# Kernel optimization log

Measured on AMD Instinct MI355X. Metric: run time of the kernel, lower is better.

Reference implementation:

```python
import jax, jax.numpy as jnp
from jax import lax
import numpy as np

B, T, MEL, H, H2, VOCAB, K, L, TXT = 16, 1000, 80, 512, 256, 80, 5, 2, 200


def _lstm_dir(x, Wih, Whh, b):
    # x: [T, B, D]; torch gate order i, f, g, o
    def step(carry, xt):
        h, c = carry
        g = xt @ Wih.T + h @ Whh.T + b
        i, f, gg, o = jnp.split(g, 4, axis=-1)
        c = jax.nn.sigmoid(f) * c + jax.nn.sigmoid(i) * jnp.tanh(gg)
        h = jax.nn.sigmoid(o) * jnp.tanh(c)
        return (h, c), h
    n = x.shape[1]
    h0 = jnp.zeros((n, Whh.shape[-1]), x.dtype)
    _, hs = lax.scan(step, (h0, h0), x)
    return hs


def _bilstm(x, Wih, Whh, b):
    # Wih: [L, 2, 4*H2, D], Whh: [L, 2, 4*H2, H2], b: [L, 2, 4*H2] (b_ih + b_hh folded)
    for l in range(Wih.shape[0]):
        fwd = _lstm_dir(x, Wih[l, 0], Whh[l, 0], b[l, 0])
        bwd = _lstm_dir(x[::-1], Wih[l, 1], Whh[l, 1], b[l, 1])[::-1]
        x = jnp.concatenate([fwd, bwd], axis=-1)
    return x


def _causal_conv(x, w, bias, pad):
    y = lax.conv_general_dilated(x, w, window_strides=(1,), padding=[(pad, 0)],
                                 dimension_numbers=('NCH', 'OIH', 'NCH'))
    return y + bias[None, :, None]


def _bn(x, g, b, m, v):
    # eval-mode BatchNorm1d over channel dim of [B, C, T]
    return (x - m[None, :, None]) * (g / jnp.sqrt(v + 1e-5))[None, :, None] + b[None, :, None]


def _ln(x, g, b):
    mu = jnp.mean(x, -1, keepdims=True)
    var = jnp.var(x, -1, keepdims=True)
    return (x - mu) / jnp.sqrt(var + 1e-5) * g + b


def _forward(mels, c1w, c1b, bn1g, bn1b, bn1m, bn1v, c2w, c2b, bn2g, bn2b, bn2m, bn2v,
             eWih, eWhh, eb, elng, elnb, cWih, cWhh, cb, ctcW, btlW, lng, lnb,
             dWih, dWhh, db, melW, mel_lengths):
    t = mels.shape[2]
    # norm_spec: spec_min=-12, spec_max=0
    x = (mels + 12.0) / 12.0 * 2.0 - 1.0
    # Conv1dPrenet (causal pads, eval-mode BN)
    y = _bn(_causal_conv(x, c1w, c1b, K - 1), bn1g, bn1b, bn1m, bn1v)
    y = _bn(_causal_conv(y, c2w, c2b, K - 1), bn2g, bn2b, bn2m, bn2v)
    xs = jnp.transpose(y, (2, 0, 1))  # [T, B, H]
    # MelEncoder BiLSTM + LayerNorm -> decoder_input [T, B, H]
    h = _ln(_bilstm(xs, eWih, eWhh, eb), elng, elnb)
    # CTCDecoder
    cx = _bilstm(h, cWih, cWhh, cb)                 # raw LSTM output (returned as ctc_hidden)
    logits = jax.nn.relu(cx) @ ctcW.T               # dropout is identity in eval
    mask = (jnp.arange(t)[:, None] < mel_lengths[None, :]).astype(logits.dtype)[:, :, None]
    log_prob = jax.nn.log_softmax(logits, axis=-1) * mask
    # bottleneck: cat(decoder_input, ctc_hidden) -> linear -> LN
    bh = _ln(jnp.concatenate([h, cx], axis=-1) @ btlW.T, lng, lnb)
    # MELDecoder (note: mel_linear applied to raw LSTM output x, matching source)
    mx = _bilstm(bh, dWih, dWhh, db)
    mel = mx @ melW.T
    mel = (mel + 1.0) / 2.0 * 12.0 - 12.0           # denorm_spec
    return mel, log_prob


def setup_inputs() -> dict:
    key = jax.random.key(0)
    ks = list(jax.random.split(key, 24))
    rn = lambda k, shape, s=0.05: jax.random.normal(k, shape, jnp.float32) * s
    G = 4 * H2
    inp = {
        'mels': jax.random.uniform(ks[0], (B, MEL, T), jnp.float32, -12.0, 0.0),
        'c1w': rn(ks[1], (H, MEL, K)), 'c1b': jnp.zeros((H,), jnp.float32),
        'bn1g': jnp.ones((H,), jnp.float32), 'bn1b': jnp.zeros((H,), jnp.float32),
        'bn1m': jnp.zeros((H,), jnp.float32), 'bn1v': jnp.ones((H,), jnp.float32),
        'c2w': rn(ks[2], (H, H, K)), 'c2b': jnp.zeros((H,), jnp.float32),
        'bn2g': jnp.ones((H,), jnp.float32), 'bn2b': jnp.zeros((H,), jnp.float32),
        'bn2m': jnp.zeros((H,), jnp.float32), 'bn2v': jnp.ones((H,), jnp.float32),
        'eWih': rn(ks[3], (L, 2, G, H)), 'eWhh': rn(ks[4], (L, 2, G, H2)), 'eb': rn(ks[5], (L, 2, G)),
        'elng': jnp.ones((H,), jnp.float32), 'elnb': jnp.zeros((H,), jnp.float32),
        'cWih': rn(ks[6], (L, 2, G, H)), 'cWhh': rn(ks[7], (L, 2, G, H2)), 'cb': rn(ks[8], (L, 2, G)),
        'ctcW': rn(ks[9], (VOCAB, H)),
        'btlW': rn(ks[10], (H, 2 * H)),
        'lng': jnp.ones((H,), jnp.float32), 'lnb': jnp.zeros((H,), jnp.float32),
        'dWih': rn(ks[11], (L, 2, G, H)), 'dWhh': rn(ks[12], (L, 2, G, H2)), 'db': rn(ks[13], (L, 2, G)),
        'melW': rn(ks[14], (MEL, H)),
        'mel_lengths': jnp.full((B,), T, jnp.int32),  # full lengths: pack/pad is identity
        'text_inputs': jax.random.randint(ks[15], (B, TXT), 0, VOCAB),
        'text_lengths': jnp.full((B,), TXT, jnp.int32),
    }
    return inp


def reference(mels, c1w, c1b, bn1g, bn1b, bn1m, bn1v, c2w, c2b, bn2g, bn2b, bn2m, bn2v,
              eWih, eWhh, eb, elng, elnb, cWih, cWhh, cb, ctcW, btlW, lng, lnb,
              dWih, dWhh, db, melW, mel_lengths, text_inputs, text_lengths):
    return _forward(mels, c1w, c1b, bn1g, bn1b, bn1m, bn1v, c2w, c2b, bn2g, bn2b, bn2m, bn2v,
                    eWih, eWhh, eb, elng, elnb, cWih, cWhh, cb, ctcW, btlW, lng, lnb,
                    dWih, dWhh, db, melW, mel_lengths)
```

## Files before the change

kernel.cpp:

```cpp
#include <hip/hip_runtime.h>
#include <hip/hip_fp16.h>


typedef unsigned int u32;
typedef _Float16 h2_t __attribute__((ext_vector_type(2)));
typedef _Float16 f16x8 __attribute__((ext_vector_type(8)));
typedef float f32x4 __attribute__((ext_vector_type(4)));
union U32H2 { u32 u; h2_t h; };

#define T_LEN 1000
#define BATCH 16
#define SROWS (T_LEN * BATCH)

__device__ __forceinline__ float dot2f(u32 a, u32 b, float c) {
#if __has_builtin(__builtin_amdgcn_fdot2)
    U32H2 ua; ua.u = a; U32H2 ub; ub.u = b;
    return __builtin_amdgcn_fdot2(ua.h, ub.h, c, false);
#else
    U32H2 ua; ua.u = a; U32H2 ub; ub.u = b;
    return c + (float)ua.h.x * (float)ub.h.x + (float)ua.h.y * (float)ub.h.y;
#endif
}

__device__ __forceinline__ u32 pack2h(float a, float b) {
    h2_t p; p.x = (_Float16)a; p.y = (_Float16)b;
    U32H2 u; u.h = p; return u.u;
}

__device__ __forceinline__ float fsigm(float x) { return 1.0f / (1.0f + __expf(-x)); }
__device__ __forceinline__ float ftanh_(float x) {
    x = fminf(fmaxf(x, -15.0f), 15.0f);
    float e = __expf(-2.0f * x);
    return (1.0f - e) / (1.0f + e);
}

__global__ void transpose_kernel(const float* __restrict__ src, float* __restrict__ dst,
                                 int R, int C) {
    int total = R * C;
    for (int i = blockIdx.x * blockDim.x + threadIdx.x; i < total; i += gridDim.x * blockDim.x) {
        int r = i / C, c = i - r * C;
        dst[(size_t)c * R + r] = src[i];
    }
}

__global__ void prep_whh_kernel(const float* __restrict__ whh, u32* __restrict__ wp, int total) {
    for (int idx = blockIdx.x * blockDim.x + threadIdx.x; idx < total; idx += gridDim.x * blockDim.x) {
        int q = idx & 3;
        int j = (idx >> 2) & 1023;
        int g = (idx >> 12) & 31;
        int d = (idx >> 17) & 1;
        int l = idx >> 18;
        int k = g * 8 + q * 2;
        const float* s = whh + ((size_t)(l * 2 + d) * 1024 + j) * 256 + k;
        wp[idx] = pack2h(s[0], s[1]);
    }
}

__global__ void pack_b_kernel(const float* __restrict__ src, _Float16* __restrict__ dst,
                              int N, int K, int sn, int sk, int off) {
    int total = N * K;
    int kst = K >> 5;
    for (int idx = blockIdx.x * blockDim.x + threadIdx.x; idx < total; idx += gridDim.x * blockDim.x) {
        int i = idx & 7;
        int lane = (idx >> 3) & 63;
        int rest = idx >> 9;
        int ks = rest % kst;
        int nt = rest / kst;
        int n = nt * 16 + (lane & 15);
        int k = ks * 32 + (lane >> 4) * 8 + i;
        dst[idx] = (_Float16)src[(size_t)n * sn + (size_t)k * sk + off];
    }
}

__global__ __launch_bounds__(256) void conv1_kernel(
    const float* __restrict__ mels, const float* __restrict__ w,
    const float* __restrict__ cbias, const float* __restrict__ bg,
    const float* __restrict__ bb, const float* __restrict__ bm,
    const float* __restrict__ bv, float* __restrict__ y1)
{
    __shared__ float xin[80 * 72];
    int t0 = blockIdx.x * 64;
    int b = blockIdx.y;
    int tid = threadIdx.x;
    for (int idx = tid; idx < 80 * 68; idx += 256) {
        int m = idx / 68, i = idx - m * 68;
        int t = t0 - 4 + i;
        float v = 0.0f;
        if (t >= 0 && t < T_LEN) v = mels[(size_t)(b * 80 + m) * T_LEN + t] * (1.0f / 6.0f) + 1.0f;
        xin[m * 72 + i] = v;
    }
    __syncthreads();
    int tg = tid & 15, cl = tid >> 4;
    for (int pass = 0; pass < 32; ++pass) {
        int c = pass * 16 + cl;
        const float* wc = w + (size_t)c * 400;
        float a0 = 0, a1 = 0, a2 = 0, a3 = 0;
        for (int m = 0; m < 80; ++m) {
            float4 xa = *(const float4*)&xin[m * 72 + tg * 4];
            float4 xb = *(const float4*)&xin[m * 72 + tg * 4 + 4];
            float w0 = wc[m * 5 + 0], w1 = wc[m * 5 + 1], w2 = wc[m * 5 + 2];
            float w3 = wc[m * 5 + 3], w4 = wc[m * 5 + 4];
            a0 += w0 * xa.x + w1 * xa.y + w2 * xa.z + w3 * xa.w + w4 * xb.x;
            a1 += w0 * xa.y + w1 * xa.z + w2 * xa.w + w3 * xb.x + w4 * xb.y;
            a2 += w0 * xa.z + w1 * xa.w + w2 * xb.x + w3 * xb.y + w4 * xb.z;
            a3 += w0 * xa.w + w1 * xb.x + w2 * xb.y + w3 * xb.z + w4 * xb.w;
        }
        float scale = bg[c] * rsqrtf(bv[c] + 1e-5f);
        float shift = (cbias[c] - bm[c]) * scale + bb[c];
        int tb = t0 + tg * 4;
        float* yp = y1 + (size_t)(b * 512 + c) * T_LEN + tb;
        if (tb + 0 < T_LEN) yp[0] = a0 * scale + shift;
        if (tb + 1 < T_LEN) yp[1] = a1 * scale + shift;
        if (tb + 2 < T_LEN) yp[2] = a2 * scale + shift;
        if (tb + 3 < T_LEN) yp[3] = a3 * scale + shift;
    }
}

__global__ __launch_bounds__(256) void relayout_kernel(
    const float* __restrict__ y1, _Float16* __restrict__ dst)
{
    __shared__ float tile[64][65];
    int t0 = blockIdx.x * 64;
    int c0 = blockIdx.y * 64;
    int b = blockIdx.z;
    int tid = threadIdx.x;
#pragma unroll
    for (int q = 0; q < 16; ++q) {
        int lin = tid + q * 256;
        int cl = lin >> 6, tl = lin & 63;
        int t = t0 + tl;
        tile[cl][tl] = (t < T_LEN) ? y1[(size_t)(b * 512 + c0 + cl) * T_LEN + t] : 0.0f;
    }
    __syncthreads();
#pragma unroll
    for (int q = 0; q < 16; ++q) {
        int lin = tid + q * 256;
        int rl = lin >> 6, cc = lin & 63;
        int t = t0 + rl;
        if (t < T_LEN)
            dst[(size_t)(t * BATCH + b) * 512 + c0 + cc] = (_Float16)tile[cc][rl];
    }
}

template<int MODE>
__global__ __launch_bounds__(512, 2) void gemm_mfma(
    const _Float16* __restrict__ A, const _Float16* __restrict__ A2, int K1,
    const uint4* __restrict__ Bp, const float* __restrict__ bias,
    float* __restrict__ C32, _Float16* __restrict__ C16,
    const float* __restrict__ cvb, const float* __restrict__ bg,
    const float* __restrict__ bb, const float* __restrict__ bm,
    const float* __restrict__ bv, int N, int K)
{
    __shared__ _Float16 At[128 * 40];
    const int m0 = blockIdx.x * 128, n0 = blockIdx.y * 128;
    const int tid = threadIdx.x, lane = tid & 63, w = tid >> 6;
    const int wm = w >> 2, wn = w & 3;
    const int srow = tid >> 2, sseg = tid & 3;
    const int ksteps = K >> 5;
    f32x4 acc[4][2];
#pragma unroll
    for (int i = 0; i < 4; ++i) { acc[i][0] = (f32x4)0.0f; acc[i][1] = (f32x4)0.0f; }

    for (int ks = 0; ks < ksteps; ++ks) {
        int k0 = ks << 5;
        uint4 av;
        if (MODE == 1) {
            int kph = k0 >> 9, kk = k0 & 511;
            int rsrc = m0 + srow + (kph - 4) * 16;
            if (rsrc >= 0) av = *(const uint4*)(A + (size_t)rsrc * 512 + kk + sseg * 8);
            else { av.x = av.y = av.z = av.w = 0u; }
        } else {
            int col = k0 + sseg * 8;
            const _Float16* src = (col < K1) ? (A + (size_t)(m0 + srow) * K1 + col)
                                             : (A2 + (size_t)(m0 + srow) * (K - K1) + (col - K1));
            av = *(const uint4*)src;
        }
        __syncthreads();
        *(uint4*)&At[srow * 40 + sseg * 8] = av;
        __syncthreads();

        f16x8 bf[2];
#pragma unroll
        for (int ct = 0; ct < 2; ++ct) {
            int nt = (n0 >> 4) + wn * 2 + ct;
            int bblk = (MODE == 1) ? ((ks >> 4) * 512 + nt * 16 + (ks & 15))
                                   : (nt * ksteps + ks);
            uint4 braw = Bp[(size_t)bblk * 64 + lane];
            bf[ct] = *(f16x8*)&braw;
        }
#pragma unroll
        for (int rt = 0; rt < 4; ++rt) {
            f16x8 af = *(f16x8*)&At[(wm * 64 + rt * 16 + (lane & 15)) * 40 + (lane >> 4) * 8];
            acc[rt][0] = __builtin_amdgcn_mfma_f32_16x16x32_f16(af, bf[0], acc[rt][0], 0, 0, 0);
            acc[rt][1] = __builtin_amdgcn_mfma_f32_16x16x32_f16(af, bf[1], acc[rt][1], 0, 0, 0);
        }
    }

    const int r0 = m0 + wm * 64 + (lane >> 4) * 4;
    const int cb0 = n0 + wn * 32 + (lane & 15);
#pragma unroll
    for (int ct = 0; ct < 2; ++ct) {
        int col = cb0 + ct * 16;
        float badd = 0.0f, sc = 0.0f, sh = 0.0f;
        if (MODE == 0) { if (bias) badd = bias[col]; }
        else {
            sc = bg[col] * rsqrtf(bv[col] + 1e-5f);
            sh = (cvb[col] - bm[col]) * sc + bb[col];
        }
#pragma unroll
        for (int rt = 0; rt < 4; ++rt) {
#pragma unroll
            for (int rr = 0; rr < 4; ++rr) {
                int row = r0 + rt * 16 + rr;
                float v = acc[rt][ct][rr];
                if (MODE == 0) C32[(size_t)row * N + col] = v + badd;
                else           C16[(size_t)row * 512 + col] = (_Float16)(v * sc + sh);
            }
        }
    }
}

#define SCAN_LDS (147456 + 4096 + 512)
__global__ __launch_bounds__(512, 2) void lstm_scan(
    const float* __restrict__ pre, const uint4* __restrict__ WPl,
    float* __restrict__ out32, _Float16* __restrict__ out16)
{
    const int b = blockIdx.x >> 1;
    const int dir = blockIdx.x & 1;
    const int tid = threadIdx.x;
    const int j0 = tid, j1 = tid + 512;

    extern __shared__ char smem[];
    uint4* w_lds = (uint4*)smem;
    float* gates = (float*)(smem + 147456);
    u32* h16 = (u32*)(smem + 147456 + 4096);

    const uint4* wp = WPl + (size_t)dir * 32768;

    for (int i = tid; i < 9216; i += 512) w_lds[i] = wp[i];

    uint4 wr0[21], wr1[21];
#pragma unroll
    for (int i = 0; i < 21; ++i) {
        wr0[i] = wp[(9 + i) * 1024 + j0];
        wr1[i] = wp[(9 + i) * 1024 + j1];
    }
    if (tid < 128) h16[tid] = 0u;
    float c = 0.0f;
    __syncthreads();

    for (int step = 0; step < T_LEN; ++step) {
        int tt = dir ? (T_LEN - 1 - step) : step;
        const float* prow = pre + (size_t)(tt * BATCH + b) * 2048 + (dir << 10);
        float acc0 = prow[j0];
        float acc1 = prow[j1];
        uint4 ws0[2], ws1[2];
#pragma unroll
        for (int i = 0; i < 2; ++i) {
            ws0[i] = wp[(30 + i) * 1024 + j0];
            ws1[i] = wp[(30 + i) * 1024 + j1];
        }
#pragma unroll
        for (int g = 0; g < 9; ++g) {
            uint4 hv = *(const uint4*)&h16[g * 4];
            uint4 w0 = w_lds[g * 1024 + j0];
            uint4 w1 = w_lds[g * 1024 + j1];
            acc0 = dot2f(hv.x, w0.x, acc0); acc0 = dot2f(hv.y, w0.y, acc0);
            acc0 = dot2f(hv.z, w0.z, acc0); acc0 = dot2f(hv.w, w0.w, acc0);
            acc1 = dot2f(hv.x, w1.x, acc1); acc1 = dot2f(hv.y, w1.y, acc1);
            acc1 = dot2f(hv.z, w1.z, acc1); acc1 = dot2f(hv.w, w1.w, acc1);
        }
#pragma unroll
        for (int i = 0; i < 21; ++i) {
            uint4 hv = *(const uint4*)&h16[(9 + i) * 4];
            acc0 = dot2f(hv.x, wr0[i].x, acc0); acc0 = dot2f(hv.y, wr0[i].y, acc0);
            acc0 = dot2f(hv.z, wr0[i].z, acc0); acc0 = dot2f(hv.w, wr0[i].w, acc0);
            acc1 = dot2f(hv.x, wr1[i].x, acc1); acc1 = dot2f(hv.y, wr1[i].y, acc1);
            acc1 = dot2f(hv.z, wr1[i].z, acc1); acc1 = dot2f(hv.w, wr1[i].w, acc1);
        }
#pragma unroll
        for (int i = 0; i < 2; ++i) {
            uint4 hv = *(const uint4*)&h16[(30 + i) * 4];
            acc0 = dot2f(hv.x, ws0[i].x, acc0); acc0 = dot2f(hv.y, ws0[i].y, acc0);
            acc0 = dot2f(hv.z, ws0[i].z, acc0); acc0 = dot2f(hv.w, ws0[i].w, acc0);
            acc1 = dot2f(hv.x, ws1[i].x, acc1); acc1 = dot2f(hv.y, ws1[i].y, acc1);
            acc1 = dot2f(hv.z, ws1[i].z, acc1); acc1 = dot2f(hv.w, ws1[i].w, acc1);
        }
        gates[j0] = acc0;
        gates[j1] = acc1;
        __syncthreads();
        if (tid < 256) {
            float gi = gates[tid], gf = gates[tid + 256];
            float gg = gates[tid + 512], go = gates[tid + 768];
            c = fsigm(gf) * c + fsigm(gi) * ftanh_(gg);
            float h = fsigm(go) * ftanh_(c);
            size_t orow = (size_t)(tt * BATCH + b) * 512 + dir * 256 + tid;
            if (out32) out32[orow] = h;
            if (out16) out16[orow] = (_Float16)h;
            float hn = __shfl_xor(h, 1);
            if ((tid & 1) == 0) h16[tid >> 1] = pack2h(h, hn);
        }
        __syncthreads();
    }
}

__global__ __launch_bounds__(256) void ln_kernel(
    const float* __restrict__ in, const float* __restrict__ g,
    const float* __restrict__ b, _Float16* __restrict__ out, int rows)
{
    int row = blockIdx.x * 4 + (threadIdx.x >> 6);
    if (row >= rows) return;
    int lane = threadIdx.x & 63;
    const float4* x = (const float4*)(in + (size_t)row * 512);
    float4 v0 = x[lane * 2], v1 = x[lane * 2 + 1];
    float s = v0.x + v0.y + v0.z + v0.w + v1.x + v1.y + v1.z + v1.w;
    float sq = v0.x * v0.x + v0.y * v0.y + v0.z * v0.z + v0.w * v0.w
             + v1.x * v1.x + v1.y * v1.y + v1.z * v1.z + v1.w * v1.w;
#pragma unroll
    for (int m = 1; m < 64; m <<= 1) {
        s += __shfl_xor(s, m);
        sq += __shfl_xor(sq, m);
    }
    float mu = s * (1.0f / 512.0f);
    float var = sq * (1.0f / 512.0f) - mu * mu;
    float rs = rsqrtf(var + 1e-5f);
    const float4* g4 = (const float4*)g;
    const float4* b4 = (const float4*)b;
    f16x8 r;
    float vv[8] = {v0.x, v0.y, v0.z, v0.w, v1.x, v1.y, v1.z, v1.w};
    float4 gg0 = g4[lane * 2], gg1 = g4[lane * 2 + 1];
    float4 bb0 = b4[lane * 2], bb1 = b4[lane * 2 + 1];
    float gA[8] = {gg0.x, gg0.y, gg0.z, gg0.w, gg1.x, gg1.y, gg1.z, gg1.w};
    float bA[8] = {bb0.x, bb0.y, bb0.z, bb0.w, bb1.x, bb1.y, bb1.z, bb1.w};
#pragma unroll
    for (int q = 0; q < 8; ++q) r[q] = (_Float16)((vv[q] - mu) * rs * gA[q] + bA[q]);
    *(f16x8*)&out[(size_t)row * 512 + lane * 8] = r;
}

__global__ __launch_bounds__(128) void ctc_head_kernel(
    const float* __restrict__ cx, const float* __restrict__ ctcWt,
    const int* __restrict__ lens, float* __restrict__ out)
{
    int r = blockIdx.x;
    int t = r / BATCH, b = r - t * BATCH;
    int tid = threadIdx.x;
    __shared__ float xr[512];
    __shared__ float red[128];
    for (int i = tid; i < 512; i += 128) xr[i] = fmaxf(cx[(size_t)r * 512 + i], 0.0f);
    __syncthreads();
    float logit = 0.0f;
    if (tid < 80) {
#pragma unroll 8
        for (int k = 0; k < 512; ++k) logit += xr[k] * ctcWt[k * 80 + tid];
    }
    red[tid] = (tid < 80) ? logit : -1e30f;
    __syncthreads();
    for (int off = 64; off > 0; off >>= 1) {
        if (tid < off) red[tid] = fmaxf(red[tid], red[tid + off]);
        __syncthreads();
    }
    float m = red[0];
    __syncthreads();
    red[tid] = (tid < 80) ? __expf(logit - m) : 0.0f;
    __syncthreads();
    for (int off = 64; off > 0; off >>= 1) {
        if (tid < off) red[tid] += red[tid + off];
        __syncthreads();
    }
    float lsum = __logf(red[0]);
    if (tid < 80) {
        float lp = logit - m - lsum;
        out[(size_t)r * 80 + tid] = (t < lens[b]) ? lp : 0.0f;
    }
}

__global__ __launch_bounds__(128) void mel_head_kernel(
    const float* __restrict__ mx, const float* __restrict__ melWt,
    float* __restrict__ out)
{
    int r = blockIdx.x;
    int tid = threadIdx.x;
    __shared__ float xr[512];
    for (int i = tid; i < 512; i += 128) xr[i] = mx[(size_t)r * 512 + i];
    __syncthreads();
    if (tid < 80) {
        float acc = 0.0f;
#pragma unroll 8
        for (int k = 0; k < 512; ++k) acc += xr[k] * melWt[k * 80 + tid];
        out[(size_t)r * 80 + tid] = acc * 6.0f - 6.0f;
    }
}

extern "C" void kernel_launch(void* const* d_in, const int* in_sizes, int n_in,
                              void* d_out, int out_size, void* d_ws, size_t ws_size,
                              hipStream_t stream) {
    const float* mels = (const float*)d_in[0];
    const float* c1w = (const float*)d_in[1];
    const float* c1b = (const float*)d_in[2];
    const float* bn1g = (const float*)d_in[3];
    const float* bn1b = (const float*)d_in[4];
    const float* bn1m = (const float*)d_in[5];
    const float* bn1v = (const float*)d_in[6];
    const float* c2w = (const float*)d_in[7];
    const float* c2b = (const float*)d_in[8];
    const float* bn2g = (const float*)d_in[9];
    const float* bn2b = (const float*)d_in[10];
    const float* bn2m = (const float*)d_in[11];
    const float* bn2v = (const float*)d_in[12];
    const float* eWih = (const float*)d_in[13];
    const float* eWhh = (const float*)d_in[14];
    const float* eb   = (const float*)d_in[15];
    const float* elng = (const float*)d_in[16];
    const float* elnb = (const float*)d_in[17];
    const float* cWih = (const float*)d_in[18];
    const float* cWhh = (const float*)d_in[19];
    const float* cb   = (const float*)d_in[20];
    const float* ctcW = (const float*)d_in[21];
    const float* btlW = (const float*)d_in[22];
    const float* lng  = (const float*)d_in[23];
    const float* lnb  = (const float*)d_in[24];
    const float* dWih = (const float*)d_in[25];
    const float* dWhh = (const float*)d_in[26];
    const float* db   = (const float*)d_in[27];
    const float* melW = (const float*)d_in[28];
    const int* mel_lengths = (const int*)d_in[29];

    float* out = (float*)d_out;
    float* ws = (float*)d_ws;

    float* preB = ws;
    float* s32  = ws + 32768000;
    _Float16* f0 = (_Float16*)(ws + 40960000);
    _Float16* f1 = f0 + 8192000;
    _Float16* f2 = f1 + 8192000;
    _Float16* f3 = f2 + 8192000;
    _Float16* BP    = f3 + 8192000;
    _Float16* BPbtl = BP + 6ull * 1048576;
    _Float16* BPcv  = BPbtl + 524288;
    u32* wpAll = (u32*)(BPcv + 5ull * 262144);
    float* ctcT = (float*)(wpAll + 6ull * 262144);
    float* melT = ctcT + 40960;

    (void)hipFuncSetAttribute((const void*)lstm_scan,
                              hipFuncAttributeMaxDynamicSharedMemorySize, SCAN_LDS);

    transpose_kernel<<<160, 256, 0, stream>>>(ctcW, ctcT, 80, 512);
    transpose_kernel<<<160, 256, 0, stream>>>(melW, melT, 80, 512);
    prep_whh_kernel<<<2048, 256, 0, stream>>>(eWhh, wpAll + 0ull * 262144, 2 * 262144);
    prep_whh_kernel<<<2048, 256, 0, stream>>>(cWhh, wpAll + 2ull * 262144, 2 * 262144);
    prep_whh_kernel<<<2048, 256, 0, stream>>>(dWhh, wpAll + 4ull * 262144, 2 * 262144);
    for (int l = 0; l < 2; ++l) {
        pack_b_kernel<<<1024, 256, 0, stream>>>(eWih + (size_t)l * 1048576,
                                                BP + (size_t)(0 + l) * 1048576, 2048, 512, 512, 1, 0);
        pack_b_kernel<<<1024, 256, 0, stream>>>(cWih + (size_t)l * 1048576,
                                                BP + (size_t)(2 + l) * 1048576, 2048, 512, 512, 1, 0);
        pack_b_kernel<<<1024, 256, 0, stream>>>(dWih + (size_t)l * 1048576,
                                                BP + (size_t)(4 + l) * 1048576, 2048, 512, 512, 1, 0);
    }
    pack_b_kernel<<<1024, 256, 0, stream>>>(btlW, BPbtl, 512, 1024, 1024, 1, 0);
    for (int kph = 0; kph < 5; ++kph)
        pack_b_kernel<<<512, 256, 0, stream>>>(c2w, BPcv + (size_t)kph * 262144,
                                               512, 512, 2560, 5, kph);

    conv1_kernel<<<dim3(16, 16), 256, 0, stream>>>(mels, c1w, c1b, bn1g, bn1b, bn1m, bn1v, s32);
    relayout_kernel<<<dim3(16, 8, 16), 256, 0, stream>>>(s32, f0);
    gemm_mfma<1><<<dim3(125, 4), 512, 0, stream>>>(f0, nullptr, 0, (const uint4*)BPcv, nullptr,
                                                   nullptr, f1, c2b, bn2g, bn2b, bn2m, bn2v, 512, 2560);

    dim3 gN2048(125, 16), gN512(125, 4);
    const uint4* BPu = (const uint4*)BP;
    gemm_mfma<0><<<gN2048, 512, 0, stream>>>(f1, nullptr, 512, BPu + 0ull * 131072, eb,
                                             preB, nullptr, nullptr, nullptr, nullptr, nullptr, nullptr, 2048, 512);
    lstm_scan<<<32, 512, SCAN_LDS, stream>>>(preB, (const uint4*)(wpAll + 0ull * 262144), nullptr, f2);
    gemm_mfma<0><<<gN2048, 512, 0, stream>>>(f2, nullptr, 512, BPu + 1ull * 131072, eb + 2048,
                                             preB, nullptr, nullptr, nullptr, nullptr, nullptr, nullptr, 2048, 512);
    lstm_scan<<<32, 512, SCAN_LDS, stream>>>(preB, (const uint4*)(wpAll + 1ull * 262144), s32, nullptr);
    ln_kernel<<<4000, 256, 0, stream>>>(s32, elng, elnb, f2, SROWS);
    gemm_mfma<0><<<gN2048, 512, 0, stream>>>(f2, nullptr, 512, BPu + 2ull * 131072, cb,
                                             preB, nullptr, nullptr, nullptr, nullptr, nullptr, nullptr, 2048, 512);
    lstm_scan<<<32, 512, SCAN_LDS, stream>>>(preB, (const uint4*)(wpAll + 2ull * 262144), nullptr, f3);
    gemm_mfma<0><<<gN2048, 512, 0, stream>>>(f3, nullptr, 512, BPu + 3ull * 131072, cb + 2048,
                                             preB, nullptr, nullptr, nullptr, nullptr, nullptr, nullptr, 2048, 512);
    lstm_scan<<<32, 512, SCAN_LDS, stream>>>(preB, (const uint4*)(wpAll + 3ull * 262144), s32, f1);
    ctc_head_kernel<<<SROWS, 128, 0, stream>>>(s32, ctcT, mel_lengths, out + (size_t)SROWS * 80);
    gemm_mfma<0><<<gN512, 512, 0, stream>>>(f2, f1, 512, (const uint4*)BPbtl, nullptr,
                                            preB, nullptr, nullptr, nullptr, nullptr, nullptr, nullptr, 512, 1024);
    ln_kernel<<<4000, 256, 0, stream>>>(preB, lng, lnb, f3, SROWS);
    gemm_mfma<0><<<gN2048, 512, 0, stream>>>(f3, nullptr, 512, BPu + 4ull * 131072, db,
                                             preB, nullptr, nullptr, nullptr, nullptr, nullptr, nullptr, 2048, 512);
    lstm_scan<<<32, 512, SCAN_LDS, stream>>>(preB, (const uint4*)(wpAll + 4ull * 262144), nullptr, f2);
    gemm_mfma<0><<<gN2048, 512, 0, stream>>>(f2, nullptr, 512, BPu + 5ull * 131072, db + 2048,
                                             preB, nullptr, nullptr, nullptr, nullptr, nullptr, nullptr, 2048, 512);
    lstm_scan<<<32, 512, SCAN_LDS, stream>>>(preB, (const uint4*)(wpAll + 5ull * 262144), s32, nullptr);
    mel_head_kernel<<<SROWS, 128, 0, stream>>>(s32, melT, out);
}
```

Baseline: 12.48 ms.

## Cache LSTM recurrent weights in AGPRs and prefetch next-step gate inputs

Moves 16 of the register-cached weight groups into accumulation VGPRs via inline asm and keeps 7 groups streamed from global memory per step. The thread-to-gate mapping changes so each thread in the lower half already holds the i and f gates, which shrinks the LDS gate exchange to only the g and o values. It also prefetches the next timestep's precomputed input projection. The aim is to relieve VGPR pressure and cut per-step LDS and global latency on the serial recurrence, at the cost of extra accvgpr read instructions and more global weight loads per step.

```diff
diff --git a/kernel.cpp b/kernel.cpp
--- a/kernel.cpp
+++ b/kernel.cpp
@@ -220,85 +220,149 @@
     }
 }
 
-#define SCAN_LDS (147456 + 4096 + 512)
-__global__ __launch_bounds__(512, 2) void lstm_scan(
+#define SCAN_LDS (147456 + 512 + 2048)
+
+#define ACLOBS \
+  "a0","a1","a2","a3","a4","a5","a6","a7","a8","a9","a10","a11","a12","a13","a14","a15", \
+  "a16","a17","a18","a19","a20","a21","a22","a23","a24","a25","a26","a27","a28","a29","a30","a31", \
+  "a32","a33","a34","a35","a36","a37","a38","a39","a40","a41","a42","a43","a44","a45","a46","a47", \
+  "a48","a49","a50","a51","a52","a53","a54","a55","a56","a57","a58","a59","a60","a61","a62","a63", \
+  "a64","a65","a66","a67","a68","a69","a70","a71","a72","a73","a74","a75","a76","a77","a78","a79", \
+  "a80","a81","a82","a83","a84","a85","a86","a87","a88","a89","a90","a91","a92","a93","a94","a95", \
+  "a96","a97","a98","a99","a100","a101","a102","a103","a104","a105","a106","a107","a108","a109","a110","a111", \
+  "a112","a113","a114","a115","a116","a117","a118","a119","a120","a121","a122","a123","a124","a125","a126","a127"
+
+#define AST(i0,i1,i2,i3, V) \
+    asm volatile("v_accvgpr_write_b32 a" #i0 ", %0\n\t" \
+                 "v_accvgpr_write_b32 a" #i1 ", %1\n\t" \
+                 "v_accvgpr_write_b32 a" #i2 ", %2\n\t" \
+                 "v_accvgpr_write_b32 a" #i3 ", %3" \
+                 :: "v"((V).x), "v"((V).y), "v"((V).z), "v"((V).w) : ACLOBS)
+
+#define ARD(N, D) asm volatile("v_accvgpr_read_b32 %0, a" #N : "=v"(D))
+
+#define STAGE2(kg, A0,A1,A2,A3, B0,B1,B2,B3) { \
+    uint4 t0_ = wp[(kg) * 1024 + r0]; AST(A0,A1,A2,A3, t0_); \
+    uint4 t1_ = wp[(kg) * 1024 + r1]; AST(B0,B1,B2,B3, t1_); }
+
+#define AGRP(kg, A0,A1,A2,A3, B0,B1,B2,B3) { \
+    uint4 hv = h4[kg]; \
+    u32 ta0,ta1,ta2,ta3,tb0,tb1,tb2,tb3; \
+    ARD(A0,ta0); ARD(A1,ta1); ARD(A2,ta2); ARD(A3,ta3); \
+    ARD(B0,tb0); ARD(B1,tb1); ARD(B2,tb2); ARD(B3,tb3); \
+    acc0 = dot2f(hv.x,ta0,acc0); acc0 = dot2f(hv.y,ta1,acc0); \
+    acc0 = dot2f(hv.z,ta2,acc0); acc0 = dot2f(hv.w,ta3,acc0); \
+    acc1 = dot2f(hv.x,tb0,acc1); acc1 = dot2f(hv.y,tb1,acc1); \
+    acc1 = dot2f(hv.z,tb2,acc1); acc1 = dot2f(hv.w,tb3,acc1); }
+
+#define SG7(M) M(25) M(26) M(27) M(28) M(29) M(30) M(31)
+
+__global__ __launch_bounds__(512) __attribute__((amdgpu_waves_per_eu(2, 2)))
+void lstm_scan(
     const float* __restrict__ pre, const uint4* __restrict__ WPl,
     float* __restrict__ out32, _Float16* __restrict__ out16)
 {
     const int b = blockIdx.x >> 1;
     const int dir = blockIdx.x & 1;
     const int tid = threadIdx.x;
-    const int j0 = tid, j1 = tid + 512;
+    const int half = tid >> 8;
+    const int j = tid & 255;
+    const int r0 = half * 512 + j;
+    const int r1 = half * 512 + 256 + j;
 
     extern __shared__ char smem[];
-    uint4* w_lds = (uint4*)smem;
-    float* gates = (float*)(smem + 147456);
-    u32* h16 = (u32*)(smem + 147456 + 4096);
+    uint4* wl = (uint4*)smem;
+    uint4* h4 = (uint4*)(smem + 147456);
+    float* gx = (float*)(smem + 147456 + 512);
 
     const uint4* wp = WPl + (size_t)dir * 32768;
 
-    for (int i = tid; i < 9216; i += 512) w_lds[i] = wp[i];
-
-    uint4 wr0[21], wr1[21];
-#pragma unroll
-    for (int i = 0; i < 21; ++i) {
-        wr0[i] = wp[(9 + i) * 1024 + j0];
-        wr1[i] = wp[(9 + i) * 1024 + j1];
-    }
+    for (int i = tid; i < 9216; i += 512) wl[i] = wp[i];
+
+    STAGE2(9,   0,1,2,3,     4,5,6,7)
+    STAGE2(10,  8,9,10,11,   12,13,14,15)
+    STAGE2(11,  16,17,18,19, 20,21,22,23)
+    STAGE2(12,  24,25,26,27, 28,29,30,31)
+    STAGE2(13,  32,33,34,35, 36,37,38,39)
+    STAGE2(14,  40,41,42,43, 44,45,46,47)
+    STAGE2(15,  48,49,50,51, 52,53,54,55)
+    STAGE2(16,  56,57,58,59, 60,61,62,63)
+    STAGE2(17,  64,65,66,67, 68,69,70,71)
+    STAGE2(18,  72,73,74,75, 76,77,78,79)
+    STAGE2(19,  80,81,82,83, 84,85,86,87)
+    STAGE2(20,  88,89,90,91, 92,93,94,95)
+    STAGE2(21,  96,97,98,99, 100,101,102,103)
+    STAGE2(22,  104,105,106,107, 108,109,110,111)
+    STAGE2(23,  112,113,114,115, 116,117,118,119)
+    STAGE2(24,  120,121,122,123, 124,125,126,127)
+
+    u32* h16 = (u32*)h4;
     if (tid < 128) h16[tid] = 0u;
     float c = 0.0f;
     __syncthreads();
 
+    int tt0 = dir ? (T_LEN - 1) : 0;
+    const float* pr0 = pre + (size_t)(tt0 * BATCH + b) * 2048 + (dir << 10);
+    float p0 = pr0[r0], p1 = pr0[r1];
+
     for (int step = 0; step < T_LEN; ++step) {
+        asm volatile("" ::: ACLOBS);
         int tt = dir ? (T_LEN - 1 - step) : step;
-        const float* prow = pre + (size_t)(tt * BATCH + b) * 2048 + (dir << 10);
-        float acc0 = prow[j0];
-        float acc1 = prow[j1];
-        uint4 ws0[2], ws1[2];
-#pragma unroll
-        for (int i = 0; i < 2; ++i) {
-            ws0[i] = wp[(30 + i) * 1024 + j0];
-            ws1[i] = wp[(30 + i) * 1024 + j1];
-        }
+        float acc0 = p0, acc1 = p1;
+        if (step + 1 < T_LEN) {
+            int tn = dir ? (T_LEN - 2 - step) : (step + 1);
+            const float* pn = pre + (size_t)(tn * BATCH + b) * 2048 + (dir << 10);
+            p0 = pn[r0]; p1 = pn[r1];
+        }
+#define DECLS(kg) uint4 sa##kg = wp[kg * 1024 + r0]; uint4 sb##kg = wp[kg * 1024 + r1];
+        SG7(DECLS)
+#undef DECLS
 #pragma unroll
         for (int g = 0; g < 9; ++g) {
-            uint4 hv = *(const uint4*)&h16[g * 4];
-            uint4 w0 = w_lds[g * 1024 + j0];
-            uint4 w1 = w_lds[g * 1024 + j1];
+            uint4 hv = h4[g];
+            uint4 w0 = wl[g * 1024 + r0];
+            uint4 w1 = wl[g * 1024 + r1];
             acc0 = dot2f(hv.x, w0.x, acc0); acc0 = dot2f(hv.y, w0.y, acc0);
             acc0 = dot2f(hv.z, w0.z, acc0); acc0 = dot2f(hv.w, w0.w, acc0);
             acc1 = dot2f(hv.x, w1.x, acc1); acc1 = dot2f(hv.y, w1.y, acc1);
             acc1 = dot2f(hv.z, w1.z, acc1); acc1 = dot2f(hv.w, w1.w, acc1);
         }
-#pragma unroll
-        for (int i = 0; i < 21; ++i) {
-            uint4 hv = *(const uint4*)&h16[(9 + i) * 4];
-            acc0 = dot2f(hv.x, wr0[i].x, acc0); acc0 = dot2f(hv.y, wr0[i].y, acc0);
-            acc0 = dot2f(hv.z, wr0[i].z, acc0); acc0 = dot2f(hv.w, wr0[i].w, acc0);
-            acc1 = dot2f(hv.x, wr1[i].x, acc1); acc1 = dot2f(hv.y, wr1[i].y, acc1);
-            acc1 = dot2f(hv.z, wr1[i].z, acc1); acc1 = dot2f(hv.w, wr1[i].w, acc1);
-        }
-#pragma unroll
-        for (int i = 0; i < 2; ++i) {
-            uint4 hv = *(const uint4*)&h16[(30 + i) * 4];
-            acc0 = dot2f(hv.x, ws0[i].x, acc0); acc0 = dot2f(hv.y, ws0[i].y, acc0);
-            acc0 = dot2f(hv.z, ws0[i].z, acc0); acc0 = dot2f(hv.w, ws0[i].w, acc0);
-            acc1 = dot2f(hv.x, ws1[i].x, acc1); acc1 = dot2f(hv.y, ws1[i].y, acc1);
-            acc1 = dot2f(hv.z, ws1[i].z, acc1); acc1 = dot2f(hv.w, ws1[i].w, acc1);
-        }
-        gates[j0] = acc0;
-        gates[j1] = acc1;
+        AGRP(9,   0,1,2,3,     4,5,6,7)
+        AGRP(10,  8,9,10,11,   12,13,14,15)
+        AGRP(11,  16,17,18,19, 20,21,22,23)
+        AGRP(12,  24,25,26,27, 28,29,30,31)
+        AGRP(13,  32,33,34,35, 36,37,38,39)
+        AGRP(14,  40,41,42,43, 44,45,46,47)
+        AGRP(15,  48,49,50,51, 52,53,54,55)
+        AGRP(16,  56,57,58,59, 60,61,62,63)
+        AGRP(17,  64,65,66,67, 68,69,70,71)
+        AGRP(18,  72,73,74,75, 76,77,78,79)
+        AGRP(19,  80,81,82,83, 84,85,86,87)
+        AGRP(20,  88,89,90,91, 92,93,94,95)
+        AGRP(21,  96,97,98,99, 100,101,102,103)
+        AGRP(22,  104,105,106,107, 108,109,110,111)
+        AGRP(23,  112,113,114,115, 116,117,118,119)
+        AGRP(24,  120,121,122,123, 124,125,126,127)
+#define USES(kg) { uint4 hv = h4[kg]; \
+        acc0 = dot2f(hv.x, sa##kg.x, acc0); acc0 = dot2f(hv.y, sa##kg.y, acc0); \
+        acc0 = dot2f(hv.z, sa##kg.z, acc0); acc0 = dot2f(hv.w, sa##kg.w, acc0); \
+        acc1 = dot2f(hv.x, sb##kg.x, acc1); acc1 = dot2f(hv.y, sb##kg.y, acc1); \
+        acc1 = dot2f(hv.z, sb##kg.z, acc1); acc1 = dot2f(hv.w, sb##kg.w, acc1); }
+        SG7(USES)
+#undef USES
+
+        if (half) { gx[j * 2] = acc0; gx[j * 2 + 1] = acc1; }
         __syncthreads();
-        if (tid < 256) {
-            float gi = gates[tid], gf = gates[tid + 256];
-            float gg = gates[tid + 512], go = gates[tid + 768];
-            c = fsigm(gf) * c + fsigm(gi) * ftanh_(gg);
+        if (!half) {
+            float gi_ = acc0, gf = acc1;
+            float gg = gx[j * 2], go = gx[j * 2 + 1];
+            c = fsigm(gf) * c + fsigm(gi_) * ftanh_(gg);
             float h = fsigm(go) * ftanh_(c);
-            size_t orow = (size_t)(tt * BATCH + b) * 512 + dir * 256 + tid;
+            size_t orow = (size_t)(tt * BATCH + b) * 512 + dir * 256 + j;
             if (out32) out32[orow] = h;
             if (out16) out16[orow] = (_Float16)h;
             float hn = __shfl_xor(h, 1);
-            if ((tid & 1) == 0) h16[tid >> 1] = pack2h(h, hn);
+            if ((j & 1) == 0) h16[j >> 1] = pack2h(h, hn);
         }
         __syncthreads();
     }
```

Result: slower. 17.92 ms (+43.6%).

## Store recurrent LSTM weights as 8-bit e5m2 streamed from global memory

Applied to the files above, without the earlier changes.

Splits the recurrent weight matrix: the first 64 input columns stay fp16 in LDS, and the remaining 192 columns become 8-bit e5m2-like values (fp16 rounded to the top byte). These are reloaded from global/L2 every step and expanded to fp16 with shifts and masks before the dot2 instructions. This removes the large register-resident weight arrays and the per-step global fp16 weight loads, and it also prefetches the next step's pre-activation row. The cost is reduced weight precision in the recurrent path, which may hurt numerical accuracy, plus extra bit-manipulation ALU work and per-step global traffic.

```diff
diff --git a/kernel.cpp b/kernel.cpp
--- a/kernel.cpp
+++ b/kernel.cpp
@@ -53,6 +53,26 @@
         int k = g * 8 + q * 2;
         const float* s = whh + ((size_t)(l * 2 + d) * 1024 + j) * 256 + k;
         wp[idx] = pack2h(s[0], s[1]);
+    }
+}
+
+__device__ __forceinline__ u32 e5b(float f) {
+    union { _Float16 h; unsigned short u; } v; v.h = (_Float16)f;
+    unsigned short r = (unsigned short)(v.u + 0x80);
+    return (u32)(r >> 8) & 0xFFu;
+}
+__global__ void prep_se5_kernel(const float* __restrict__ whh, u32* __restrict__ sp, int total) {
+    for (int idx = blockIdx.x * blockDim.x + threadIdx.x; idx < total; idx += gridDim.x * blockDim.x) {
+        int c = idx & 3;
+        int row = (idx >> 2) & 1023;
+        int rest = idx >> 12;
+        int p = rest % 12;
+        int ld = rest / 12;
+        int kg = 8 + 2 * p + (c >> 1);
+        int k0 = kg * 8 + (c & 1) * 4;
+        const float* s = whh + ((size_t)ld * 1024 + row) * 256 + k0;
+        u32 v = (e5b(s[3]) << 24) | (e5b(s[1]) << 16) | (e5b(s[2]) << 8) | e5b(s[0]);
+        sp[idx] = v;
     }
 }
 
@@ -220,9 +240,25 @@
     }
 }
 
-#define SCAN_LDS (147456 + 4096 + 512)
-__global__ __launch_bounds__(512, 2) void lstm_scan(
+#define SCAN_LDS (131072 + 4096 + 512)
+
+#define P12(M) M(0) M(1) M(2) M(3) M(4) M(5) M(6) M(7) M(8) M(9) M(10) M(11)
+
+#define DQDOT(U, GA, GB, ACC) { \
+    uint4 hA = h4[GA], hB = h4[GB]; \
+    u32 lo_, hi_; \
+    lo_ = (U.x << 8) & 0xFF00FF00u; hi_ = U.x & 0xFF00FF00u; \
+    ACC = dot2f(hA.x, lo_, ACC); ACC = dot2f(hA.y, hi_, ACC); \
+    lo_ = (U.y << 8) & 0xFF00FF00u; hi_ = U.y & 0xFF00FF00u; \
+    ACC = dot2f(hA.z, lo_, ACC); ACC = dot2f(hA.w, hi_, ACC); \
+    lo_ = (U.z << 8) & 0xFF00FF00u; hi_ = U.z & 0xFF00FF00u; \
+    ACC = dot2f(hB.x, lo_, ACC); ACC = dot2f(hB.y, hi_, ACC); \
+    lo_ = (U.w << 8) & 0xFF00FF00u; hi_ = U.w & 0xFF00FF00u; \
+    ACC = dot2f(hB.z, lo_, ACC); ACC = dot2f(hB.w, hi_, ACC); }
+
+__global__ __launch_bounds__(512) void lstm_scan(
     const float* __restrict__ pre, const uint4* __restrict__ WPl,
+    const uint4* __restrict__ SPl,
     float* __restrict__ out32, _Float16* __restrict__ out16)
 {
     const int b = blockIdx.x >> 1;
@@ -231,61 +267,51 @@
     const int j0 = tid, j1 = tid + 512;
 
     extern __shared__ char smem[];
-    uint4* w_lds = (uint4*)smem;
-    float* gates = (float*)(smem + 147456);
-    u32* h16 = (u32*)(smem + 147456 + 4096);
+    uint4* wl = (uint4*)smem;
+    float* gates = (float*)(smem + 131072);
+    uint4* h4 = (uint4*)(smem + 131072 + 4096);
+    u32* h16 = (u32*)h4;
 
     const uint4* wp = WPl + (size_t)dir * 32768;
-
-    for (int i = tid; i < 9216; i += 512) w_lds[i] = wp[i];
-
-    uint4 wr0[21], wr1[21];
-#pragma unroll
-    for (int i = 0; i < 21; ++i) {
-        wr0[i] = wp[(9 + i) * 1024 + j0];
-        wr1[i] = wp[(9 + i) * 1024 + j1];
-    }
+    for (int i = tid; i < 8192; i += 512) wl[i] = wp[i];
+
+    unsigned long long sb = (unsigned long long)(SPl + (size_t)dir * 12288);
+
     if (tid < 128) h16[tid] = 0u;
     float c = 0.0f;
     __syncthreads();
 
+    int tt0 = dir ? (T_LEN - 1) : 0;
+    const float* pr0 = pre + (size_t)(tt0 * BATCH + b) * 2048 + (dir << 10);
+    float p0 = pr0[j0], p1 = pr0[j1];
+
     for (int step = 0; step < T_LEN; ++step) {
+        asm("" : "+v"(sb));
+        const uint4* sp = (const uint4*)sb;
         int tt = dir ? (T_LEN - 1 - step) : step;
-        const float* prow = pre + (size_t)(tt * BATCH + b) * 2048 + (dir << 10);
-        float acc0 = prow[j0];
-        float acc1 = prow[j1];
-        uint4 ws0[2], ws1[2];
-#pragma unroll
-        for (int i = 0; i < 2; ++i) {
-            ws0[i] = wp[(30 + i) * 1024 + j0];
-            ws1[i] = wp[(30 + i) * 1024 + j1];
-        }
-#pragma unroll
-        for (int g = 0; g < 9; ++g) {
-            uint4 hv = *(const uint4*)&h16[g * 4];
-            uint4 w0 = w_lds[g * 1024 + j0];
-            uint4 w1 = w_lds[g * 1024 + j1];
+        float acc0 = p0, acc1 = p1;
+        if (step + 1 < T_LEN) {
+            int tn = dir ? (T_LEN - 2 - step) : (step + 1);
+            const float* pn = pre + (size_t)(tn * BATCH + b) * 2048 + (dir << 10);
+            p0 = pn[j0]; p1 = pn[j1];
+        }
+#define DECLS(p) uint4 sA##p = sp[p * 1024 + j0]; uint4 sB##p = sp[p * 1024 + j1];
+        P12(DECLS)
+#undef DECLS
+#pragma unroll
+        for (int g = 0; g < 8; ++g) {
+            uint4 hv = h4[g];
+            uint4 w0 = wl[g * 1024 + j0];
+            uint4 w1 = wl[g * 1024 + j1];
             acc0 = dot2f(hv.x, w0.x, acc0); acc0 = dot2f(hv.y, w0.y, acc0);
             acc0 = dot2f(hv.z, w0.z, acc0); acc0 = dot2f(hv.w, w0.w, acc0);
             acc1 = dot2f(hv.x, w1.x, acc1); acc1 = dot2f(hv.y, w1.y, acc1);
             acc1 = dot2f(hv.z, w1.z, acc1); acc1 = dot2f(hv.w, w1.w, acc1);
         }
-#pragma unroll
-        for (int i = 0; i < 21; ++i) {
-            uint4 hv = *(const uint4*)&h16[(9 + i) * 4];
-            acc0 = dot2f(hv.x, wr0[i].x, acc0); acc0 = dot2f(hv.y, wr0[i].y, acc0);
-            acc0 = dot2f(hv.z, wr0[i].z, acc0); acc0 = dot2f(hv.w, wr0[i].w, acc0);
-            acc1 = dot2f(hv.x, wr1[i].x, acc1); acc1 = dot2f(hv.y, wr1[i].y, acc1);
-            acc1 = dot2f(hv.z, wr1[i].z, acc1); acc1 = dot2f(hv.w, wr1[i].w, acc1);
-        }
-#pragma unroll
-        for (int i = 0; i < 2; ++i) {
-            uint4 hv = *(const uint4*)&h16[(30 + i) * 4];
-            acc0 = dot2f(hv.x, ws0[i].x, acc0); acc0 = dot2f(hv.y, ws0[i].y, acc0);
-            acc0 = dot2f(hv.z, ws0[i].z, acc0); acc0 = dot2f(hv.w, ws0[i].w, acc0);
-            acc1 = dot2f(hv.x, ws1[i].x, acc1); acc1 = dot2f(hv.y, ws1[i].y, acc1);
-            acc1 = dot2f(hv.z, ws1[i].z, acc1); acc1 = dot2f(hv.w, ws1[i].w, acc1);
-        }
+#define USES(p) DQDOT(sA##p, 8 + 2 * p, 9 + 2 * p, acc0) \
+                DQDOT(sB##p, 8 + 2 * p, 9 + 2 * p, acc1)
+        P12(USES)
+#undef USES
         gates[j0] = acc0;
         gates[j1] = acc1;
         __syncthreads();
@@ -440,6 +466,7 @@
     u32* wpAll = (u32*)(BPcv + 5ull * 262144);
     float* ctcT = (float*)(wpAll + 6ull * 262144);
     float* melT = ctcT + 40960;
+    u32* spAll = (u32*)(melT + 40960);
 
     (void)hipFuncSetAttribute((const void*)lstm_scan,
                               hipFuncAttributeMaxDynamicSharedMemorySize, SCAN_LDS);
@@ -449,6 +476,9 @@
     prep_whh_kernel<<<2048, 256, 0, stream>>>(eWhh, wpAll + 0ull * 262144, 2 * 262144);
     prep_whh_kernel<<<2048, 256, 0, stream>>>(cWhh, wpAll + 2ull * 262144, 2 * 262144);
     prep_whh_kernel<<<2048, 256, 0, stream>>>(dWhh, wpAll + 4ull * 262144, 2 * 262144);
+    prep_se5_kernel<<<768, 256, 0, stream>>>(eWhh, spAll + 0ull * 98304, 196608);
+    prep_se5_kernel<<<768, 256, 0, stream>>>(cWhh, spAll + 2ull * 98304, 196608);
+    prep_se5_kernel<<<768, 256, 0, stream>>>(dWhh, spAll + 4ull * 98304, 196608);
     for (int l = 0; l < 2; ++l) {
         pack_b_kernel<<<1024, 256, 0, stream>>>(eWih + (size_t)l * 1048576,
                                                 BP + (size_t)(0 + l) * 1048576, 2048, 512, 512, 1, 0);
@@ -469,28 +499,32 @@
 
     dim3 gN2048(125, 16), gN512(125, 4);
     const uint4* BPu = (const uint4*)BP;
+#define WPL(i) (const uint4*)(wpAll + (unsigned long long)(i) * 262144)
+#define SPL(i) (const uint4*)(spAll + (unsigned long long)(i) * 98304)
     gemm_mfma<0><<<gN2048, 512, 0, stream>>>(f1, nullptr, 512, BPu + 0ull * 131072, eb,
                                              preB, nullptr, nullptr, nullptr, nullptr, nullptr, nullptr, 2048, 512);
-    lstm_scan<<<32, 512, SCAN_LDS, stream>>>(preB, (const uint4*)(wpAll + 0ull * 262144), nullptr, f2);
+    lstm_scan<<<32, 512, SCAN_LDS, stream>>>(preB, WPL(0), SPL(0), nullptr, f2);
     gemm_mfma<0><<<gN2048, 512, 0, stream>>>(f2, nullptr, 512, BPu + 1ull * 131072, eb + 2048,
                                              preB, nullptr, nullptr, nullptr, nullptr, nullptr, nullptr, 2048, 512);
-    lstm_scan<<<32, 512, SCAN_LDS, stream>>>(preB, (const uint4*)(wpAll + 1ull * 262144), s32, nullptr);
+    lstm_scan<<<32, 512, SCAN_LDS, stream>>>(preB, WPL(1), SPL(1), s32, nullptr);
     ln_kernel<<<4000, 256, 0, stream>>>(s32, elng, elnb, f2, SROWS);
     gemm_mfma<0><<<gN2048, 512, 0, stream>>>(f2, nullptr, 512, BPu + 2ull * 131072, cb,
                                              preB, nullptr, nullptr, nullptr, nullptr, nullptr, nullptr, 2048, 512);
-    lstm_scan<<<32, 512, SCAN_LDS, stream>>>(preB, (const uint4*)(wpAll + 2ull * 262144), nullptr, f3);
+    lstm_scan<<<32, 512, SCAN_LDS, stream>>>(preB, WPL(2), SPL(2), nullptr, f3);
     gemm_mfma<0><<<gN2048, 512, 0, stream>>>(f3, nullptr, 512, BPu + 3ull * 131072, cb + 2048,
                                              preB, nullptr, nullptr, nullptr, nullptr, nullptr, nullptr, 2048, 512);
-    lstm_scan<<<32, 512, SCAN_LDS, stream>>>(preB, (const uint4*)(wpAll + 3ull * 262144), s32, f1);
+    lstm_scan<<<32, 512, SCAN_LDS, stream>>>(preB, WPL(3), SPL(3), s32, f1);
     ctc_head_kernel<<<SROWS, 128, 0, stream>>>(s32, ctcT, mel_lengths, out + (size_t)SROWS * 80);
     gemm_mfma<0><<<gN512, 512, 0, stream>>>(f2, f1, 512, (const uint4*)BPbtl, nullptr,
                                             preB, nullptr, nullptr, nullptr, nullptr, nullptr, nullptr, 512, 1024);
     ln_kernel<<<4000, 256, 0, stream>>>(preB, lng, lnb, f3, SROWS);
     gemm_mfma<0><<<gN2048, 512, 0, stream>>>(f3, nullptr, 512, BPu + 4ull * 131072, db,
                                              preB, nullptr, nullptr, nullptr, nullptr, nullptr, nullptr, 2048, 512);
-    lstm_scan<<<32, 512, SCAN_LDS, stream>>>(preB, (const uint4*)(wpAll + 4ull * 262144), nullptr, f2);
+    lstm_scan<<<32, 512, SCAN_LDS, stream>>>(preB, WPL(4), SPL(4), nullptr, f2);
     gemm_mfma<0><<<gN2048, 512, 0, stream>>>(f2, nullptr, 512, BPu + 5ull * 131072, db + 2048,
                                              preB, nullptr, nullptr, nullptr, nullptr, nullptr, nullptr, 2048, 512);
-    lstm_scan<<<32, 512, SCAN_LDS, stream>>>(preB, (const uint4*)(wpAll + 5ull * 262144), s32, nullptr);
+    lstm_scan<<<32, 512, SCAN_LDS, stream>>>(preB, WPL(5), SPL(5), s32, nullptr);
     mel_head_kernel<<<SROWS, 128, 0, stream>>>(s32, melT, out);
-}
+#undef WPL
+#undef SPL
+}
```

Result: slower. 23.64 ms (+89.4%).
